# Optimization experiments

Measured on AMD Instinct MI355X. Metric: run time of the kernel, lower is better.

## Reference

```python
import jax, jax.numpy as jnp
import numpy as np

H = 2048          # hidden_size
DIN = 4096        # mamba intermediate (expand*H)
DS = 128          # ssm state size
DCONV = 4         # conv kernel
NH = 64           # ssm heads
HD = DIN // NH    # head dim = 64
NG = 1            # groups
FF = 8192         # mlp intermediate
EPS = 1e-5
B, L = 2, 2048
CONV_DIM = DIN + 2 * NG * DS            # 4352
D_IN_PROJ = 2 * DIN + 2 * NG * DS + NH  # 8512


def rmsnorm(x, w, eps=EPS):
    v = jnp.mean(jnp.square(x), axis=-1, keepdims=True)
    return x * jax.lax.rsqrt(v + eps) * w


def setup_inputs() -> dict:
    key = jax.random.key(0)
    ks = jax.random.split(key, 10)
    return {
        "hidden_states": jax.random.normal(ks[0], (B, L, H), jnp.float32),
        "w_in": 0.02 * jax.random.normal(ks[1], (H, D_IN_PROJ), jnp.float32),
        "conv_w": 0.1 * jax.random.normal(ks[2], (CONV_DIM, DCONV), jnp.float32),
        "conv_b": jnp.zeros((CONV_DIM,), jnp.float32),
        "A_log": jnp.log(1.0 + 15.0 * jax.random.uniform(ks[3], (NH,), jnp.float32)),
        "D_ssm": jnp.ones((NH,), jnp.float32),
        "dt_bias": 0.5 * jax.random.normal(ks[4], (NH,), jnp.float32),
        "norm_w": jnp.ones((DIN,), jnp.float32),
        "w_out": 0.02 * jax.random.normal(ks[5], (DIN, H), jnp.float32),
        "ln1_w": jnp.ones((H,), jnp.float32),
        "ln2_w": jnp.ones((H,), jnp.float32),
        "w_gate_up": 0.02 * jax.random.normal(ks[6], (H, 2 * FF), jnp.float32),
        "w_down": 0.02 * jax.random.normal(ks[7], (FF, H), jnp.float32),
    }


def mamba_mixer2(h, w_in, conv_w, conv_b, A_log, D_ssm, dt_bias, norm_w, w_out):
    # in_proj and split: [gate z | conv stream xBC | dt]
    proj = jnp.einsum('blh,hd->bld', h, w_in)
    z = proj[..., :DIN]
    xBC = proj[..., DIN:DIN + CONV_DIM]
    dt = proj[..., DIN + CONV_DIM:]                      # [B,L,NH]

    # causal depthwise conv over time, then silu
    kernel = conv_w.T[:, None, :]                        # [DCONV,1,CONV_DIM]
    xBC = jax.lax.conv_general_dilated(
        xBC, kernel, window_strides=(1,), padding=[(DCONV - 1, 0)],
        dimension_numbers=('NLC', 'LIO', 'NLC'), feature_group_count=CONV_DIM)
    xBC = jax.nn.silu(xBC + conv_b)

    x = xBC[..., :DIN].reshape(B, L, NH, HD)             # [B,L,NH,HD]
    Bc = xBC[..., DIN:DIN + NG * DS]                     # [B,L,DS] (NG=1)
    Cc = xBC[..., DIN + NG * DS:]                        # [B,L,DS]

    dt = jax.nn.softplus(dt + dt_bias)                   # [B,L,NH]
    A = -jnp.exp(A_log)                                  # [NH]
    dA = jnp.exp(dt * A)                                 # [B,L,NH]

    def step(hstate, inp):
        dA_t, dt_t, x_t, B_t, C_t = inp
        # hstate: [B,NH,HD,DS]
        hstate = (hstate * dA_t[:, :, None, None]
                  + (dt_t[:, :, None, None] * x_t[..., None]) * B_t[:, None, None, :])
        y_t = jnp.einsum('bhps,bs->bhp', hstate, C_t)
        return hstate, y_t

    h0 = jnp.zeros((B, NH, HD, DS), h.dtype)
    xs = (jnp.moveaxis(dA, 1, 0), jnp.moveaxis(dt, 1, 0), jnp.moveaxis(x, 1, 0),
          jnp.moveaxis(Bc, 1, 0), jnp.moveaxis(Cc, 1, 0))
    _, ys = jax.lax.scan(step, h0, xs)                   # ys: [L,B,NH,HD]
    y = jnp.moveaxis(ys, 0, 1) + D_ssm[None, None, :, None] * x
    y = y.reshape(B, L, DIN)

    # gated RMSNorm then out projection
    y = rmsnorm(y * jax.nn.silu(z), norm_w)
    return jnp.einsum('bld,dh->blh', y, w_out)


def reference(hidden_states, w_in, conv_w, conv_b, A_log, D_ssm, dt_bias,
              norm_w, w_out, ln1_w, ln2_w, w_gate_up, w_down):
    # residual is None on entry (first mamba layer path)
    residual = hidden_states
    h = rmsnorm(hidden_states, ln1_w)
    h = mamba_mixer2(h, w_in, conv_w, conv_b, A_log, D_ssm, dt_bias, norm_w, w_out)
    # fused add + norm
    residual = h + residual
    h = rmsnorm(residual, ln2_w)
    # SwiGLU MLP
    gu = jnp.einsum('blh,hf->blf', h, w_gate_up)
    h = jax.nn.silu(gu[..., :FF]) * gu[..., FF:]
    h = jnp.einsum('blf,fh->blh', h, w_down)
    return h, residual
```

## Files before the change

### kernel.cpp

```cpp
#include <hip/hip_runtime.h>
#include <hip/hip_bf16.h>
#include <stdint.h>

typedef __hip_bfloat16 bf16;
typedef __attribute__((ext_vector_type(8))) short bf16x8s;
typedef __attribute__((ext_vector_type(4))) float f32x4;
typedef __attribute__((ext_vector_type(8))) unsigned short us8;

#define DEV __device__ __forceinline__
#define MFMA16(a, b, c) __builtin_amdgcn_mfma_f32_16x16x32_bf16(a, b, c, 0, 0, 0)
#define AS1 __attribute__((address_space(1)))
#define AS3 __attribute__((address_space(3)))

static constexpr int Bn = 2, Ln = 2048, Hn = 2048, DINn = 4096, DSn = 128;
static constexpr int NHn = 64, FFn = 8192;
static constexpr int CONVD = DINn + 2 * DSn;
static constexpr int DPROJ = 2 * DINn + 2 * DSn + NHn;
static constexpr int DPROJP = 8704;
static constexpr int BL = Bn * Ln;
static constexpr int LC2 = 64, NCH = Ln / LC2;

DEV float bf2f(unsigned short x) {
  union { unsigned int u; float f; } v; v.u = ((unsigned int)x) << 16; return v.f;
}
DEV float bfload(const bf16* p) { return bf2f(*(const unsigned short*)p); }
DEV float sigmoidf_(float x) { return 1.f / (1.f + __expf(-x)); }

__global__ __launch_bounds__(256) void transpose_f2b_k(
    const float* __restrict__ in, bf16* __restrict__ out, int K, int N) {
  __shared__ bf16 t[32][33];
  int nb = blockIdx.x * 32, kb = blockIdx.y * 32;
  int tx = threadIdx.x & 31, ty = threadIdx.x >> 5;
#pragma unroll
  for (int r = 0; r < 32; r += 8)
    t[ty + r][tx] = __float2bfloat16(in[(size_t)(kb + ty + r) * N + nb + tx]);
  __syncthreads();
#pragma unroll
  for (int r = 0; r < 32; r += 8)
    out[(size_t)(nb + ty + r) * K + kb + tx] = t[tx][ty + r];
}

__global__ __launch_bounds__(256) void rmsnorm_f32_k(
    const float* __restrict__ in, const float* __restrict__ g, bf16* __restrict__ out) {
  int row = blockIdx.x, tid = threadIdx.x;
  const float* rp = in + (size_t)row * Hn + tid * 8;
  float4 a = *(const float4*)rp;
  float4 b = *(const float4*)(rp + 4);
  float v[8] = {a.x, a.y, a.z, a.w, b.x, b.y, b.z, b.w};
  float ss = 0.f;
#pragma unroll
  for (int j = 0; j < 8; ++j) ss += v[j] * v[j];
#pragma unroll
  for (int o = 1; o < 64; o <<= 1) ss += __shfl_xor(ss, o, 64);
  __shared__ float red[4];
  if ((tid & 63) == 0) red[tid >> 6] = ss;
  __syncthreads();
  float sc = rsqrtf((red[0] + red[1] + red[2] + red[3]) / Hn + 1e-5f);
  float4 g0 = *(const float4*)(g + tid * 8);
  float4 g1 = *(const float4*)(g + tid * 8 + 4);
  float gv[8] = {g0.x, g0.y, g0.z, g0.w, g1.x, g1.y, g1.z, g1.w};
  us8 ov;
#pragma unroll
  for (int j = 0; j < 8; ++j)
    ((bf16*)&ov)[j] = __float2bfloat16(v[j] * sc * gv[j]);
  *(us8*)(out + (size_t)row * Hn + tid * 8) = ov;
}

template<int MF, int EPI, typename OutT>
__global__ __launch_bounds__(512, (MF == 8 ? 2 : 4)) void gemm256_k(
    const bf16* __restrict__ A, const bf16* __restrict__ Bt,
    OutT* __restrict__ C, const float* __restrict__ Res,
    int K, int lda, int N, int nby) {
  constexpr int BM = MF * 32;
  __shared__ bf16 Abuf[3][BM * 32];
  __shared__ bf16 Bbuf[3][256 * 32];
  int nwg = gridDim.x;
  int orig = blockIdx.x;
  int wg = (orig & 7) * (nwg >> 3) + (orig >> 3);
  int by = wg % nby, bx = wg / nby;
  int m0 = by * BM, n0 = bx * 256;
  int tid = threadIdx.x;
  int lane = tid & 63, wid = tid >> 6;
  int wr = wid >> 2, wc = wid & 3;
  int l15 = lane & 15, l4 = lane >> 4;

  int P0 = tid * 16;
  int P1 = 8192 + tid * 16;
  int L0 = P0 ^ (((P0 >> 7) & 3) << 4);
  int L1 = P1 ^ (((P1 >> 7) & 3) << 4);
  int ar1 = (MF == 8) ? (L1 >> 6) : 0;
  const bf16* Ag0 = A + (size_t)(m0 + (L0 >> 6)) * lda + ((L0 >> 4) & 3) * 8;
  const bf16* Ag1 = A + (size_t)(m0 + ar1) * lda + ((L1 >> 4) & 3) * 8;
  const bf16* Bg0 = Bt + (size_t)(n0 + (L0 >> 6)) * K + ((L0 >> 4) & 3) * 8;
  const bf16* Bg1 = Bt + (size_t)(n0 + (L1 >> 6)) * K + ((L1 >> 4) & 3) * 8;

  auto stage = [&](int bi, int k0) {
    char* ab = (char*)&Abuf[bi][0];
    char* bb = (char*)&Bbuf[bi][0];
    __builtin_amdgcn_global_load_lds((const AS1 unsigned int*)(Ag0 + k0), (AS3 unsigned int*)(ab + P0), 16, 0, 0);
    if constexpr (MF == 8)
      __builtin_amdgcn_global_load_lds((const AS1 unsigned int*)(Ag1 + k0), (AS3 unsigned int*)(ab + P1), 16, 0, 0);
    __builtin_amdgcn_global_load_lds((const AS1 unsigned int*)(Bg0 + k0), (AS3 unsigned int*)(bb + P0), 16, 0, 0);
    __builtin_amdgcn_global_load_lds((const AS1 unsigned int*)(Bg1 + k0), (AS3 unsigned int*)(bb + P1), 16, 0, 0);
  };

  f32x4 acc[MF][4] = {};
  int arow0 = wr * (MF * 16) + l15;
  int acol = (l4 * 16) ^ (((arow0 >> 1) & 3) << 4);
  int brow0 = wc * 64 + l15;
  int bcol = (l4 * 16) ^ (((brow0 >> 1) & 3) << 4);
  int NT = K >> 5;

  stage(0, 0);
  stage(1, 32);
  if constexpr (MF == 8) asm volatile("s_waitcnt vmcnt(4)" ::: "memory");
  else                   asm volatile("s_waitcnt vmcnt(3)" ::: "memory");
  __builtin_amdgcn_s_barrier();
  asm volatile("" ::: "memory");

  for (int t = 0; t < NT; ++t) {
    const char* Ab = (const char*)&Abuf[t % 3][0];
    const char* Bb = (const char*)&Bbuf[t % 3][0];
    bf16x8s af[MF], bfv[4];
#pragma unroll
    for (int m = 0; m < MF; ++m)
      af[m] = *(const bf16x8s*)(Ab + (arow0 + m * 16) * 64 + acol);
#pragma unroll
    for (int n = 0; n < 4; ++n)
      bfv[n] = *(const bf16x8s*)(Bb + (brow0 + n * 16) * 64 + bcol);
    if (t + 2 < NT) stage((t + 2) % 3, (t + 2) * 32);
    __builtin_amdgcn_s_setprio(1);
#pragma unroll
    for (int m = 0; m < MF; ++m)
#pragma unroll
      for (int n = 0; n < 4; ++n)
        acc[m][n] = MFMA16(af[m], bfv[n], acc[m][n]);
    __builtin_amdgcn_s_setprio(0);
    if (t + 2 < NT) {
      if constexpr (MF == 8) asm volatile("s_waitcnt vmcnt(4)" ::: "memory");
      else                   asm volatile("s_waitcnt vmcnt(3)" ::: "memory");
    } else {
      asm volatile("s_waitcnt vmcnt(0)" ::: "memory");
    }
    __builtin_amdgcn_s_barrier();
    asm volatile("" ::: "memory");
  }

#pragma unroll
  for (int m = 0; m < MF; ++m) {
    int row = m0 + wr * (MF * 16) + m * 16 + l4 * 4;
#pragma unroll
    for (int n = 0; n < 4; ++n) {
      int col = n0 + wc * 64 + n * 16 + l15;
      if (col < N) {
#pragma unroll
        for (int r = 0; r < 4; ++r) {
          float vv = acc[m][n][r];
          if (EPI == 1) vv += Res[(size_t)(row + r) * N + col];
          if constexpr (__is_same(OutT, float)) C[(size_t)(row + r) * N + col] = vv;
          else C[(size_t)(row + r) * N + col] = __float2bfloat16(vv);
        }
      }
    }
  }
}

__global__ __launch_bounds__(256) void conv_silu_k(
    const bf16* __restrict__ proj, const float* __restrict__ cw,
    const float* __restrict__ cb, bf16* __restrict__ xb, bf16* __restrict__ bc) {
  int c = blockIdx.x * 256 + threadIdx.x;
  int bt = blockIdx.y;
  int l = bt & (Ln - 1);
  const bf16* base = proj + (size_t)bt * DPROJ + DINn + c;
  float acc = cb[c];
#pragma unroll
  for (int k = 0; k < 4; ++k) {
    int dl = l - 3 + k;
    if (dl >= 0) acc += bfload(base + (ptrdiff_t)(k - 3) * DPROJ) * cw[c * 4 + k];
  }
  float r = acc * sigmoidf_(acc);
  if (c < DINn) xb[(size_t)bt * DINn + c] = __float2bfloat16(r);
  else          bc[(size_t)bt * 256 + (c - DINn)] = __float2bfloat16(r);
}

__global__ __launch_bounds__(256) void dtda_k(
    const bf16* __restrict__ proj, const float* __restrict__ dt_bias,
    const float* __restrict__ A_log, float* __restrict__ dt, float* __restrict__ la) {
  int i = blockIdx.x * 256 + threadIdx.x;
  int bt = i >> 6, h = i & 63;
  float raw = bfload(proj + (size_t)bt * DPROJ + (DINn + CONVD) + h) + dt_bias[h];
  float dtv = raw > 20.f ? raw : log1pf(expf(raw));
  float Ah = -expf(A_log[h]);
  dt[i] = dtv;
  la[i] = dtv * Ah;
}

__global__ __launch_bounds__(256) void cumsum_k(
    const float* __restrict__ la, float* __restrict__ sarr) {
  int blk = blockIdx.x;
  int b = blk >> 6, h = blk & 63;
  int tid = threadIdx.x;
  int ch = tid >> 3, l8 = tid & 7;
  int t0 = ch * LC2 + l8 * 8;
  const float* lp = la + ((size_t)b * Ln + t0) * NHn + h;
  float v[8];
#pragma unroll
  for (int k = 0; k < 8; ++k) v[k] = lp[(size_t)k * NHn];
#pragma unroll
  for (int k = 1; k < 8; ++k) v[k] += v[k - 1];
  float tot = v[7];
  float run = tot;
#pragma unroll
  for (int d = 1; d < 8; d <<= 1) {
    float u = __shfl_up(run, d, 8);
    if (l8 >= d) run += u;
  }
  float excl = run - tot;
  float* out = sarr + (size_t)blk * Ln + t0;
#pragma unroll
  for (int k = 0; k < 8; ++k) out[k] = excl + v[k];
}

__global__ __launch_bounds__(256) void ssd1_k(
    const bf16* __restrict__ xb, const bf16* __restrict__ bc,
    const float* __restrict__ dtb, const float* __restrict__ sarr,
    bf16* __restrict__ ys, bf16* __restrict__ hend) {
  __shared__ bf16 Bs[64][136];
  __shared__ bf16 Cs[64][136];
  __shared__ bf16 BdT[128][72];
  __shared__ bf16 XTs[64][72];
  __shared__ bf16 Ss[64][72];
  __shared__ float sA[64];
  __shared__ float dts[64];
  int idx = blockIdx.x;
  int ch = idx & (NCH - 1), h = (idx >> 5) & 63, b = idx >> 11;
  int tid = threadIdx.x;
  size_t bt0 = (size_t)b * Ln + ch * LC2;
  if (tid < 64) {
    sA[tid] = sarr[(size_t)(b * 64 + h) * Ln + ch * LC2 + tid];
    dts[tid] = dtb[(bt0 + tid) * NHn + h];
  }
  __syncthreads();
  float sLast = sA[63];
  {
    int j = tid & 63, q = tid >> 6;
    float wj = dts[j] * __expf(sLast - sA[j]);
    const bf16* src = bc + (bt0 + j) * 256 + q * 64;
#pragma unroll
    for (int m8 = 0; m8 < 8; ++m8) {
      us8 v = *(const us8*)(src + m8 * 8);
      if (q < 2) {
        *(us8*)&Bs[j][q * 64 + m8 * 8] = v;
#pragma unroll
        for (int e = 0; e < 8; ++e)
          BdT[q * 64 + m8 * 8 + e][j] = __float2bfloat16(bf2f(v[e]) * wj);
      } else {
        *(us8*)&Cs[j][(q - 2) * 64 + m8 * 8] = v;
      }
    }
  }
  {
    int j = tid & 63, q = tid >> 6;
    const bf16* src = xb + (bt0 + j) * DINn + h * 64 + q * 16;
    us8 v0 = *(const us8*)src;
    us8 v1 = *(const us8*)(src + 8);
#pragma unroll
    for (int e = 0; e < 8; ++e) XTs[q * 16 + e][j] = *(const bf16*)&((unsigned short*)&v0)[e];
#pragma unroll
    for (int e = 0; e < 8; ++e) XTs[q * 16 + 8 + e][j] = *(const bf16*)&((unsigned short*)&v1)[e];
  }
  __syncthreads();
  int lane = tid & 63, wid = tid >> 6;
  int wr = wid >> 1, wc = wid & 1;
  int l15 = lane & 15, l4 = lane >> 4;
  f32x4 acc1[2][2] = {};
#pragma unroll
  for (int kk = 0; kk < 4; ++kk) {
    int kr = kk * 32 + l4 * 8;
    bf16x8s a0 = *(const bf16x8s*)&Cs[wr * 32 + l15][kr];
    bf16x8s a1 = *(const bf16x8s*)&Cs[wr * 32 + 16 + l15][kr];
    bf16x8s b0 = *(const bf16x8s*)&Bs[wc * 32 + l15][kr];
    bf16x8s b1 = *(const bf16x8s*)&Bs[wc * 32 + 16 + l15][kr];
    acc1[0][0] = MFMA16(a0, b0, acc1[0][0]);
    acc1[0][1] = MFMA16(a0, b1, acc1[0][1]);
    acc1[1][0] = MFMA16(a1, b0, acc1[1][0]);
    acc1[1][1] = MFMA16(a1, b1, acc1[1][1]);
  }
#pragma unroll
  for (int m = 0; m < 2; ++m)
#pragma unroll
    for (int n = 0; n < 2; ++n) {
      int j = wc * 32 + n * 16 + l15;
      float sj = sA[j], dj = dts[j];
#pragma unroll
      for (int r = 0; r < 4; ++r) {
        int i = wr * 32 + m * 16 + l4 * 4 + r;
        float val = (i >= j) ? __expf(sA[i] - sj) * acc1[m][n][r] * dj : 0.f;
        Ss[i][j] = __float2bfloat16(val);
      }
    }
  __syncthreads();
  f32x4 acc2[2][2] = {};
#pragma unroll
  for (int kk = 0; kk < 2; ++kk) {
    int kr = kk * 32 + l4 * 8;
    bf16x8s a0 = *(const bf16x8s*)&Ss[wr * 32 + l15][kr];
    bf16x8s a1 = *(const bf16x8s*)&Ss[wr * 32 + 16 + l15][kr];
    bf16x8s b0 = *(const bf16x8s*)&XTs[wc * 32 + l15][kr];
    bf16x8s b1 = *(const bf16x8s*)&XTs[wc * 32 + 16 + l15][kr];
    acc2[0][0] = MFMA16(a0, b0, acc2[0][0]);
    acc2[0][1] = MFMA16(a0, b1, acc2[0][1]);
    acc2[1][0] = MFMA16(a1, b0, acc2[1][0]);
    acc2[1][1] = MFMA16(a1, b1, acc2[1][1]);
  }
#pragma unroll
  for (int m = 0; m < 2; ++m)
#pragma unroll
    for (int n = 0; n < 2; ++n) {
      int p = wc * 32 + n * 16 + l15;
#pragma unroll
      for (int r = 0; r < 4; ++r) {
        int i = wr * 32 + m * 16 + l4 * 4 + r;
        ys[(bt0 + i) * DINn + h * 64 + p] = __float2bfloat16(acc2[m][n][r]);
      }
    }
  f32x4 acc3[2][4] = {};
#pragma unroll
  for (int kk = 0; kk < 2; ++kk) {
    int kr = kk * 32 + l4 * 8;
    bf16x8s a0 = *(const bf16x8s*)&XTs[wr * 32 + l15][kr];
    bf16x8s a1 = *(const bf16x8s*)&XTs[wr * 32 + 16 + l15][kr];
#pragma unroll
    for (int n = 0; n < 4; ++n) {
      bf16x8s bb = *(const bf16x8s*)&BdT[wc * 64 + n * 16 + l15][kr];
      acc3[0][n] = MFMA16(a0, bb, acc3[0][n]);
      acc3[1][n] = MFMA16(a1, bb, acc3[1][n]);
    }
  }
  bf16* hb = hend + ((size_t)((b * 64 + h) * NCH + ch)) * 8192;
#pragma unroll
  for (int m = 0; m < 2; ++m)
#pragma unroll
    for (int n = 0; n < 4; ++n) {
      int s = wc * 64 + n * 16 + l15;
#pragma unroll
      for (int r = 0; r < 4; ++r) {
        int p = wr * 32 + m * 16 + l4 * 4 + r;
        hb[p * 128 + s] = __float2bfloat16(acc3[m][n][r]);
      }
    }
}

__global__ __launch_bounds__(256) void carry_k(
    bf16* __restrict__ hend, const float* __restrict__ sarr) {
  int blk = blockIdx.x;
  int tid = threadIdx.x;
  bf16* base = hend + (size_t)blk * NCH * 8192 + tid * 32;
  const float* sp = sarr + (size_t)blk * Ln;
  float c[32];
#pragma unroll
  for (int i = 0; i < 32; ++i) c[i] = 0.f;
  for (int j = 0; j < NCH; ++j) {
    float aT = __expf(sp[j * LC2 + LC2 - 1]);
    bf16* pj = base + (size_t)j * 8192;
    float tmp[32];
#pragma unroll
    for (int q = 0; q < 4; ++q) {
      us8 v = ((const us8*)pj)[q];
#pragma unroll
      for (int e = 0; e < 8; ++e) tmp[q * 8 + e] = bf2f(v[e]);
    }
#pragma unroll
    for (int q = 0; q < 4; ++q) {
      us8 o;
#pragma unroll
      for (int e = 0; e < 8; ++e) ((bf16*)&o)[e] = __float2bfloat16(c[q * 8 + e]);
      ((us8*)pj)[q] = o;
    }
#pragma unroll
    for (int i = 0; i < 32; ++i) c[i] = fmaf(aT, c[i], tmp[i]);
  }
}

__global__ __launch_bounds__(256) void ssd2_k(
    const bf16* __restrict__ bc, const float* __restrict__ sarr,
    const bf16* __restrict__ hinit, bf16* __restrict__ ys) {
  __shared__ bf16 Ce[64][136];
  __shared__ bf16 Hs[64][136];
  __shared__ float sA[64];
  int idx = blockIdx.x;
  int ch = idx & (NCH - 1), h = (idx >> 5) & 63, b = idx >> 11;
  int tid = threadIdx.x;
  size_t bt0 = (size_t)b * Ln + ch * LC2;
  if (tid < 64) sA[tid] = sarr[(size_t)(b * 64 + h) * Ln + ch * LC2 + tid];
  __syncthreads();
  {
    int i = tid & 63, q = tid >> 6;
    float ei = __expf(sA[i]);
    const bf16* src = bc + (bt0 + i) * 256 + 128 + q * 32;
#pragma unroll
    for (int m8 = 0; m8 < 4; ++m8) {
      us8 v = *(const us8*)(src + m8 * 8);
      us8 o;
#pragma unroll
      for (int e = 0; e < 8; ++e) ((bf16*)&o)[e] = __float2bfloat16(bf2f(v[e]) * ei);
      *(us8*)&Ce[i][q * 32 + m8 * 8] = o;
    }
    const bf16* hsrc = hinit + ((size_t)((b * 64 + h) * NCH + ch)) * 8192 + i * 128 + q * 32;
#pragma unroll
    for (int m8 = 0; m8 < 4; ++m8)
      *(us8*)&Hs[i][q * 32 + m8 * 8] = *(const us8*)(hsrc + m8 * 8);
  }
  __syncthreads();
  int lane = tid & 63, wid = tid >> 6;
  int wr = wid >> 1, wc = wid & 1;
  int l15 = lane & 15, l4 = lane >> 4;
  f32x4 acc[2][2] = {};
#pragma unroll
  for (int kk = 0; kk < 4; ++kk) {
    int kr = kk * 32 + l4 * 8;
    bf16x8s a0 = *(const bf16x8s*)&Ce[wr * 32 + l15][kr];
    bf16x8s a1 = *(const bf16x8s*)&Ce[wr * 32 + 16 + l15][kr];
    bf16x8s b0 = *(const bf16x8s*)&Hs[wc * 32 + l15][kr];
    bf16x8s b1 = *(const bf16x8s*)&Hs[wc * 32 + 16 + l15][kr];
    acc[0][0] = MFMA16(a0, b0, acc[0][0]);
    acc[0][1] = MFMA16(a0, b1, acc[0][1]);
    acc[1][0] = MFMA16(a1, b0, acc[1][0]);
    acc[1][1] = MFMA16(a1, b1, acc[1][1]);
  }
#pragma unroll
  for (int m = 0; m < 2; ++m)
#pragma unroll
    for (int n = 0; n < 2; ++n) {
      int p = wc * 32 + n * 16 + l15;
#pragma unroll
      for (int r = 0; r < 4; ++r) {
        int i = wr * 32 + m * 16 + l4 * 4 + r;
        bf16* yy = &ys[(bt0 + i) * DINn + h * 64 + p];
        *yy = __float2bfloat16(bfload(yy) + acc[m][n][r]);
      }
    }
}

__global__ __launch_bounds__(256) void gated_norm_k(
    const bf16* __restrict__ ys, const bf16* __restrict__ xb,
    const float* __restrict__ Dp, const bf16* __restrict__ proj,
    const float* __restrict__ gw, bf16* __restrict__ out) {
  int row = blockIdx.x, tid = threadIdx.x;
  const bf16* yr = ys + (size_t)row * DINn;
  const bf16* xr = xb + (size_t)row * DINn;
  const bf16* zr = proj + (size_t)row * DPROJ;
  float v[2][8];
  float ss = 0.f;
#pragma unroll
  for (int it = 0; it < 2; ++it) {
    int base = (it * 256 + tid) * 8;
    float Dh = Dp[base >> 6];
    us8 y = *(const us8*)(yr + base);
    us8 x = *(const us8*)(xr + base);
    us8 z = *(const us8*)(zr + base);
#pragma unroll
    for (int j = 0; j < 8; ++j) {
      float zf = bf2f(z[j]);
      float val = (bf2f(y[j]) + Dh * bf2f(x[j])) * zf * sigmoidf_(zf);
      v[it][j] = val; ss += val * val;
    }
  }
#pragma unroll
  for (int o = 1; o < 64; o <<= 1) ss += __shfl_xor(ss, o, 64);
  __shared__ float red[4];
  if ((tid & 63) == 0) red[tid >> 6] = ss;
  __syncthreads();
  float sc = rsqrtf((red[0] + red[1] + red[2] + red[3]) / DINn + 1e-5f);
#pragma unroll
  for (int it = 0; it < 2; ++it) {
    int base = (it * 256 + tid) * 8;
    float4 g0 = *(const float4*)(gw + base);
    float4 g1 = *(const float4*)(gw + base + 4);
    float gv[8] = {g0.x, g0.y, g0.z, g0.w, g1.x, g1.y, g1.z, g1.w};
    us8 ov;
#pragma unroll
    for (int j = 0; j < 8; ++j)
      ((bf16*)&ov)[j] = __float2bfloat16(v[it][j] * sc * gv[j]);
    *(us8*)(out + (size_t)row * DINn + base) = ov;
  }
}

__global__ __launch_bounds__(256) void act_k(bf16* __restrict__ gu) {
  int i = blockIdx.x * 256 + threadIdx.x;
  int row = i >> 10, g = i & 1023;
  bf16* rp = gu + (size_t)row * (2 * FFn) + g * 8;
  us8 a = *(const us8*)(rp);
  us8 bx = *(const us8*)(rp + FFn);
  us8 ov;
#pragma unroll
  for (int j = 0; j < 8; ++j) {
    float av = bf2f(a[j]), bv = bf2f(bx[j]);
    ((bf16*)&ov)[j] = __float2bfloat16(av * sigmoidf_(av) * bv);
  }
  *(us8*)rp = ov;
}

extern "C" void kernel_launch(void* const* d_in, const int* in_sizes, int n_in,
                              void* d_out, int out_size, void* d_ws, size_t ws_size,
                              hipStream_t stream) {
  (void)in_sizes; (void)n_in; (void)out_size; (void)ws_size;
  const float* hidden  = (const float*)d_in[0];
  const float* w_in    = (const float*)d_in[1];
  const float* conv_w  = (const float*)d_in[2];
  const float* conv_b  = (const float*)d_in[3];
  const float* A_log   = (const float*)d_in[4];
  const float* D_ssm   = (const float*)d_in[5];
  const float* dt_bias = (const float*)d_in[6];
  const float* norm_w  = (const float*)d_in[7];
  const float* w_out   = (const float*)d_in[8];
  const float* ln1_w   = (const float*)d_in[9];
  const float* ln2_w   = (const float*)d_in[10];
  const float* w_gu    = (const float*)d_in[11];
  const float* w_dn    = (const float*)d_in[12];

  char* ws = (char*)d_ws;
  const size_t OFF_WT   = 0;
  const size_t OFF_PROJ = 67108864ull;
  const size_t OFF_XB   = OFF_PROJ + 69730304ull;
  const size_t OFF_BC   = OFF_XB  + 33554432ull;
  const size_t OFF_DTB  = OFF_BC  + 2097152ull;
  const size_t OFF_LA   = OFF_DTB + 1048576ull;
  const size_t OFF_SARR = OFF_LA  + 1048576ull;
  const size_t OFF_YS   = OFF_SARR + 1048576ull;
  const size_t OFF_YBF  = OFF_YS  + 33554432ull;
  const size_t OFF_HLN  = OFF_YBF + 33554432ull;
  const size_t OFF_HEND = OFF_WT;
  const size_t OFF_GU   = OFF_PROJ;

  bf16*  wT   = (bf16*)(ws + OFF_WT);
  bf16*  proj = (bf16*)(ws + OFF_PROJ);
  bf16*  xb   = (bf16*)(ws + OFF_XB);
  bf16*  bcb  = (bf16*)(ws + OFF_BC);
  float* dtb  = (float*)(ws + OFF_DTB);
  float* la   = (float*)(ws + OFF_LA);
  float* sarr = (float*)(ws + OFF_SARR);
  bf16*  ysb  = (bf16*)(ws + OFF_YS);
  bf16*  ybf  = (bf16*)(ws + OFF_YBF);
  bf16*  hln  = (bf16*)(ws + OFF_HLN);
  bf16*  hend = (bf16*)(ws + OFF_HEND);
  bf16*  gu   = (bf16*)(ws + OFF_GU);

  float* h_out = (float*)d_out;
  float* resid = h_out + (size_t)BL * Hn;

  transpose_f2b_k<<<dim3(DPROJ / 32, Hn / 32), 256, 0, stream>>>(w_in, wT, Hn, DPROJ);
  hipMemsetAsync(wT + (size_t)DPROJ * Hn, 0, (size_t)(DPROJP - DPROJ) * Hn * 2, stream);
  rmsnorm_f32_k<<<BL, 256, 0, stream>>>(hidden, ln1_w, hln);
  gemm256_k<8, 0, bf16><<<(DPROJP / 256) * (BL / 256), 512, 0, stream>>>(
      hln, wT, proj, nullptr, Hn, Hn, DPROJ, BL / 256);

  conv_silu_k<<<dim3(CONVD / 256, BL), 256, 0, stream>>>(proj, conv_w, conv_b, xb, bcb);
  dtda_k<<<BL * NHn / 256, 256, 0, stream>>>(proj, dt_bias, A_log, dtb, la);
  cumsum_k<<<Bn * NHn, 256, 0, stream>>>(la, sarr);

  ssd1_k<<<Bn * NHn * NCH, 256, 0, stream>>>(xb, bcb, dtb, sarr, ysb, hend);
  carry_k<<<Bn * NHn, 256, 0, stream>>>(hend, sarr);
  ssd2_k<<<Bn * NHn * NCH, 256, 0, stream>>>(bcb, sarr, hend, ysb);

  gated_norm_k<<<BL, 256, 0, stream>>>(ysb, xb, D_ssm, proj, norm_w, ybf);
  transpose_f2b_k<<<dim3(Hn / 32, DINn / 32), 256, 0, stream>>>(w_out, wT, DINn, Hn);
  gemm256_k<4, 1, float><<<(Hn / 256) * (BL / 128), 512, 0, stream>>>(
      ybf, wT, resid, hidden, DINn, DINn, Hn, BL / 128);

  rmsnorm_f32_k<<<BL, 256, 0, stream>>>(resid, ln2_w, hln);
  transpose_f2b_k<<<dim3(2 * FFn / 32, Hn / 32), 256, 0, stream>>>(w_gu, wT, Hn, 2 * FFn);
  gemm256_k<8, 0, bf16><<<(2 * FFn / 256) * (BL / 256), 512, 0, stream>>>(
      hln, wT, gu, nullptr, Hn, Hn, 2 * FFn, BL / 256);
  act_k<<<BL * FFn / 8 / 256, 256, 0, stream>>>(gu);
  transpose_f2b_k<<<dim3(Hn / 32, FFn / 32), 256, 0, stream>>>(w_dn, wT, FFn, Hn);
  gemm256_k<4, 0, float><<<(Hn / 256) * (BL / 128), 512, 0, stream>>>(
      gu, wT, h_out, nullptr, FFn, 2 * FFn, Hn, BL / 128);
}
```

Measured before the change: 1.048 ms.

## Add 256x256 GEMM with K=64 double-buffered, XOR-swizzled LDS and interleaved staging

Adds a new 256x256 tile GEMM kernel that loads K=64 slices into two LDS buffers split into half-tiles, using direct global-to-LDS loads and an XOR swizzle to avoid bank conflicts. Each K step is split into four MFMA quadrants, and the next tile's half-loads are issued between them so global traffic overlaps the matrix math. It replaces the triple-buffered K=32 kernel for the in_proj and gate_up GEMMs, the two largest bf16-output matmuls. It adds many barriers and depends on careful vmcnt accounting, so a counting mistake could cause races or stalls.

```diff
diff --git a/kernel.cpp b/kernel.cpp
--- a/kernel.cpp
+++ b/kernel.cpp
@@ -64,6 +64,152 @@
   for (int j = 0; j < 8; ++j)
     ((bf16*)&ov)[j] = __float2bfloat16(v[j] * sc * gv[j]);
   *(us8*)(out + (size_t)row * Hn + tid * 8) = ov;
+}
+
+template<int EPI, typename OutT>
+__global__ __launch_bounds__(512, 2) void gemm8p_k(
+    const bf16* __restrict__ A, const bf16* __restrict__ Bt,
+    OutT* __restrict__ C, const float* __restrict__ Res,
+    int K, int lda, int N, int nby) {
+  __shared__ bf16 Ab[2][2][128 * 64];
+  __shared__ bf16 Bb[2][2][128 * 64];
+  int nwg = gridDim.x;
+  int orig = blockIdx.x;
+  int wg = (orig & 7) * (nwg >> 3) + (orig >> 3);
+  int by = wg % nby, bx = wg / nby;
+  int m0 = by * 256, n0 = bx * 256;
+  int tid = threadIdx.x;
+  int lane = tid & 63, wid = tid >> 6;
+  int wr = wid >> 2, wc = wid & 3;
+  int l15 = lane & 15, l4 = lane >> 4;
+  int NT = K >> 6;
+
+  int P0 = tid * 16, P1 = tid * 16 + 8192;
+  int r0 = P0 >> 7, r1 = P1 >> 7;
+  int s0 = ((P0 >> 4) & 7) ^ (r0 & 7);
+  int s1 = ((P1 >> 4) & 7) ^ (r1 & 7);
+  const bf16* Ag[2][2];
+  const bf16* Bg[2][2];
+#pragma unroll
+  for (int h = 0; h < 2; ++h) {
+    Ag[h][0] = A + (size_t)(m0 + h * 128 + r0) * lda + s0 * 8;
+    Ag[h][1] = A + (size_t)(m0 + h * 128 + r1) * lda + s1 * 8;
+    Bg[h][0] = Bt + (size_t)(n0 + h * 128 + r0) * K + s0 * 8;
+    Bg[h][1] = Bt + (size_t)(n0 + h * 128 + r1) * K + s1 * 8;
+  }
+
+  auto stageA = [&](int t) {
+  };
+  (void)stageA;
+#define STAGE_A(hh, tt)                                                                  \
+  if ((tt) < NT) {                                                                       \
+    char* dst = (char*)&Ab[(tt) & 1][hh][0];                                             \
+    __builtin_amdgcn_global_load_lds((const AS1 unsigned int*)(Ag[hh][0] + (tt) * 64),   \
+                                     (AS3 unsigned int*)(dst + P0), 16, 0, 0);           \
+    __builtin_amdgcn_global_load_lds((const AS1 unsigned int*)(Ag[hh][1] + (tt) * 64),   \
+                                     (AS3 unsigned int*)(dst + P1), 16, 0, 0);           \
+  }
+#define STAGE_B(hh, tt)                                                                  \
+  if ((tt) < NT) {                                                                       \
+    char* dst = (char*)&Bb[(tt) & 1][hh][0];                                             \
+    __builtin_amdgcn_global_load_lds((const AS1 unsigned int*)(Bg[hh][0] + (tt) * 64),   \
+                                     (AS3 unsigned int*)(dst + P0), 16, 0, 0);           \
+    __builtin_amdgcn_global_load_lds((const AS1 unsigned int*)(Bg[hh][1] + (tt) * 64),   \
+                                     (AS3 unsigned int*)(dst + P1), 16, 0, 0);           \
+  }
+
+  f32x4 acc[8][4] = {};
+  bf16x8s af[4], bf[4];
+
+#define LDA_FRAG(i, mh, kk, d)                                                            \
+  {                                                                                       \
+    int rr = (mh) * 64 + (i) * 16 + l15;                                                  \
+    af[i] = *(const bf16x8s*)((const char*)&Ab[d][wr][0] + rr * 128 +                     \
+                              ((((kk) * 4 + l4) ^ (rr & 7)) << 4));                       \
+  }
+#define LDB_FRAG(n, kk, d)                                                                \
+  {                                                                                       \
+    int rr = (wc & 1) * 64 + (n) * 16 + l15;                                              \
+    bf[n] = *(const bf16x8s*)((const char*)&Bb[d][wc >> 1][0] + rr * 128 +                \
+                              ((((kk) * 4 + l4) ^ (rr & 7)) << 4));                       \
+  }
+#define MFMA_QUAD(mh, kk)                                                                 \
+  __builtin_amdgcn_s_setprio(1);                                                         \
+  _Pragma("unroll") for (int i = 0; i < 4; ++i) {                                        \
+    _Pragma("unroll") for (int n = 0; n < 4; ++n)                                        \
+        acc[(mh) * 4 + i][n] = MFMA16(af[i], bf[n], acc[(mh) * 4 + i][n]);               \
+  }                                                                                       \
+  __builtin_amdgcn_s_setprio(0);
+#define LGKM0                                                                             \
+  asm volatile("s_waitcnt lgkmcnt(0)" ::: "memory");                                      \
+  __builtin_amdgcn_sched_barrier(0);
+
+  STAGE_A(0, 0) STAGE_A(1, 0) STAGE_B(0, 0) STAGE_B(1, 0) STAGE_B(0, 1)
+  if (NT > 1) { asm volatile("s_waitcnt vmcnt(2)" ::: "memory"); }
+  else        { asm volatile("s_waitcnt vmcnt(0)" ::: "memory"); }
+  __builtin_amdgcn_s_barrier();
+
+  for (int t = 0; t < NT; ++t) {
+    const int d = t & 1;
+#pragma unroll
+    for (int i = 0; i < 4; ++i) LDA_FRAG(i, 0, 0, d)
+#pragma unroll
+    for (int n = 0; n < 4; ++n) LDB_FRAG(n, 0, d)
+    STAGE_B(1, t + 1)
+    __builtin_amdgcn_s_barrier();
+    LGKM0
+    MFMA_QUAD(0, 0)
+    __builtin_amdgcn_s_barrier();
+#pragma unroll
+    for (int i = 0; i < 4; ++i) LDA_FRAG(i, 1, 0, d)
+    STAGE_A(0, t + 1)
+    __builtin_amdgcn_s_barrier();
+    LGKM0
+    MFMA_QUAD(1, 0)
+    __builtin_amdgcn_s_barrier();
+#pragma unroll
+    for (int i = 0; i < 4; ++i) LDA_FRAG(i, 0, 1, d)
+#pragma unroll
+    for (int n = 0; n < 4; ++n) LDB_FRAG(n, 1, d)
+    STAGE_A(1, t + 1)
+    __builtin_amdgcn_s_barrier();
+    LGKM0
+    MFMA_QUAD(0, 1)
+    __builtin_amdgcn_s_barrier();
+#pragma unroll
+    for (int i = 0; i < 4; ++i) LDA_FRAG(i, 1, 1, d)
+    STAGE_B(0, t + 2)
+    __builtin_amdgcn_s_barrier();
+    LGKM0
+    MFMA_QUAD(1, 1)
+    if (t + 2 < NT) { asm volatile("s_waitcnt vmcnt(2)" ::: "memory"); }
+    else            { asm volatile("s_waitcnt vmcnt(0)" ::: "memory"); }
+    __builtin_amdgcn_s_barrier();
+  }
+
+#pragma unroll
+  for (int m = 0; m < 8; ++m) {
+    int row = m0 + wr * 128 + m * 16 + l4 * 4;
+#pragma unroll
+    for (int n = 0; n < 4; ++n) {
+      int col = n0 + wc * 64 + n * 16 + l15;
+      if (col < N) {
+#pragma unroll
+        for (int r = 0; r < 4; ++r) {
+          float vv = acc[m][n][r];
+          if (EPI == 1) vv += Res[(size_t)(row + r) * N + col];
+          if constexpr (__is_same(OutT, float)) C[(size_t)(row + r) * N + col] = vv;
+          else C[(size_t)(row + r) * N + col] = __float2bfloat16(vv);
+        }
+      }
+    }
+  }
+#undef STAGE_A
+#undef STAGE_B
+#undef LDA_FRAG
+#undef LDB_FRAG
+#undef MFMA_QUAD
+#undef LGKM0
 }
 
 template<int MF, int EPI, typename OutT>
@@ -552,7 +698,7 @@
   transpose_f2b_k<<<dim3(DPROJ / 32, Hn / 32), 256, 0, stream>>>(w_in, wT, Hn, DPROJ);
   hipMemsetAsync(wT + (size_t)DPROJ * Hn, 0, (size_t)(DPROJP - DPROJ) * Hn * 2, stream);
   rmsnorm_f32_k<<<BL, 256, 0, stream>>>(hidden, ln1_w, hln);
-  gemm256_k<8, 0, bf16><<<(DPROJP / 256) * (BL / 256), 512, 0, stream>>>(
+  gemm8p_k<0, bf16><<<(DPROJP / 256) * (BL / 256), 512, 0, stream>>>(
       hln, wT, proj, nullptr, Hn, Hn, DPROJ, BL / 256);
 
   conv_silu_k<<<dim3(CONVD / 256, BL), 256, 0, stream>>>(proj, conv_w, conv_b, xb, bcb);
@@ -570,7 +716,7 @@
 
   rmsnorm_f32_k<<<BL, 256, 0, stream>>>(resid, ln2_w, hln);
   transpose_f2b_k<<<dim3(2 * FFn / 32, Hn / 32), 256, 0, stream>>>(w_gu, wT, Hn, 2 * FFn);
-  gemm256_k<8, 0, bf16><<<(2 * FFn / 256) * (BL / 256), 512, 0, stream>>>(
+  gemm8p_k<0, bf16><<<(2 * FFn / 256) * (BL / 256), 512, 0, stream>>>(
       hln, wT, gu, nullptr, Hn, Hn, 2 * FFn, BL / 256);
   act_k<<<BL * FFn / 8 / 256, 256, 0, stream>>>(gu);
   transpose_f2b_k<<<dim3(Hn / 32, FFn / 32), 256, 0, stream>>>(w_dn, wT, FFn, Hn);
```

Result: no change. 1.069 ms (+1.9%).

## Add GEMM variant loading B fragments directly into registers, bypassing LDS

Applied to the files above, without the earlier changes.

Adds a 256x256 GEMM kernel that stages only the A tile through LDS with triple buffering. Each wave loads its B-operand fragments straight from global memory into registers, double-buffered across K steps. It is used for the in-projection and gate/up GEMMs. This halves LDS traffic and LDS footprint per block, but makes B loads uncoalesced across lanes (each lane reads 16 bytes from a different row) and repeats B reads across the two wave rows.

```diff
diff --git a/kernel.cpp b/kernel.cpp
--- a/kernel.cpp
+++ b/kernel.cpp
@@ -64,6 +64,118 @@
   for (int j = 0; j < 8; ++j)
     ((bf16*)&ov)[j] = __float2bfloat16(v[j] * sc * gv[j]);
   *(us8*)(out + (size_t)row * Hn + tid * 8) = ov;
+}
+
+template<int EPI, typename OutT>
+__global__ __launch_bounds__(512, 2) void gemmBreg_k(
+    const bf16* __restrict__ A, const bf16* __restrict__ Bt,
+    OutT* __restrict__ C, const float* __restrict__ Res,
+    int K, int lda, int N, int nby) {
+  __shared__ bf16 Abuf[3][256 * 32];
+  int nwg = gridDim.x;
+  int orig = blockIdx.x;
+  int wg = (orig & 7) * (nwg >> 3) + (orig >> 3);
+  int by = wg % nby, bx = wg / nby;
+  int m0 = by * 256, n0 = bx * 256;
+  int tid = threadIdx.x;
+  int lane = tid & 63, wid = tid >> 6;
+  int wr = wid >> 2, wc = wid & 3;
+  int l15 = lane & 15, l4 = lane >> 4;
+
+  int P0 = tid * 16;
+  int P1 = 8192 + tid * 16;
+  int L0 = P0 ^ (((P0 >> 7) & 3) << 4);
+  int L1 = P1 ^ (((P1 >> 7) & 3) << 4);
+  const bf16* Ag0 = A + (size_t)(m0 + (L0 >> 6)) * lda + ((L0 >> 4) & 3) * 8;
+  const bf16* Ag1 = A + (size_t)(m0 + (L1 >> 6)) * lda + ((L1 >> 4) & 3) * 8;
+
+  auto stageA = [&](int bi, int k0) {
+    char* ab = (char*)&Abuf[bi][0];
+    __builtin_amdgcn_global_load_lds((const AS1 unsigned int*)(Ag0 + k0), (AS3 unsigned int*)(ab + P0), 16, 0, 0);
+    __builtin_amdgcn_global_load_lds((const AS1 unsigned int*)(Ag1 + k0), (AS3 unsigned int*)(ab + P1), 16, 0, 0);
+  };
+
+  const bf16* Bp[4];
+#pragma unroll
+  for (int n = 0; n < 4; ++n)
+    Bp[n] = Bt + (size_t)(n0 + wc * 64 + n * 16 + l15) * K + l4 * 8;
+
+  f32x4 acc[8][4] = {};
+  int arow0 = wr * 128 + l15;
+  int acol = (l4 * 16) ^ (((arow0 >> 1) & 3) << 4);
+  int NT = K >> 5;
+
+  bf16x8s bA[4], bB[4], af[8];
+
+  stageA(0, 0);
+#pragma unroll
+  for (int n = 0; n < 4; ++n) bA[n] = *(const bf16x8s*)(Bp[n]);
+  stageA(1, 32);
+  asm volatile("s_waitcnt vmcnt(2)" ::: "memory");
+  __builtin_amdgcn_s_barrier();
+
+  for (int t = 0; t < NT; t += 2) {
+    {
+      const char* Ab = (const char*)&Abuf[t % 3][0];
+#pragma unroll
+      for (int m = 0; m < 8; ++m)
+        af[m] = *(const bf16x8s*)(Ab + (arow0 + m * 16) * 64 + acol);
+      if (t + 1 < NT) {
+#pragma unroll
+        for (int n = 0; n < 4; ++n) bB[n] = *(const bf16x8s*)(Bp[n] + (t + 1) * 32);
+      }
+      if (t + 2 < NT) stageA((t + 2) % 3, (t + 2) * 32);
+      __builtin_amdgcn_s_setprio(1);
+#pragma unroll
+      for (int m = 0; m < 8; ++m)
+#pragma unroll
+        for (int n = 0; n < 4; ++n)
+          acc[m][n] = MFMA16(af[m], bA[n], acc[m][n]);
+      __builtin_amdgcn_s_setprio(0);
+      if (t + 2 < NT) { asm volatile("s_waitcnt vmcnt(2)" ::: "memory"); }
+      else            { asm volatile("s_waitcnt vmcnt(0)" ::: "memory"); }
+      __builtin_amdgcn_s_barrier();
+    }
+    if (t + 1 < NT) {
+      const char* Ab = (const char*)&Abuf[(t + 1) % 3][0];
+#pragma unroll
+      for (int m = 0; m < 8; ++m)
+        af[m] = *(const bf16x8s*)(Ab + (arow0 + m * 16) * 64 + acol);
+      if (t + 2 < NT) {
+#pragma unroll
+        for (int n = 0; n < 4; ++n) bA[n] = *(const bf16x8s*)(Bp[n] + (t + 2) * 32);
+      }
+      if (t + 3 < NT) stageA((t + 3) % 3, (t + 3) * 32);
+      __builtin_amdgcn_s_setprio(1);
+#pragma unroll
+      for (int m = 0; m < 8; ++m)
+#pragma unroll
+        for (int n = 0; n < 4; ++n)
+          acc[m][n] = MFMA16(af[m], bB[n], acc[m][n]);
+      __builtin_amdgcn_s_setprio(0);
+      if (t + 3 < NT) { asm volatile("s_waitcnt vmcnt(2)" ::: "memory"); }
+      else            { asm volatile("s_waitcnt vmcnt(0)" ::: "memory"); }
+      __builtin_amdgcn_s_barrier();
+    }
+  }
+
+#pragma unroll
+  for (int m = 0; m < 8; ++m) {
+    int row = m0 + wr * 128 + m * 16 + l4 * 4;
+#pragma unroll
+    for (int n = 0; n < 4; ++n) {
+      int col = n0 + wc * 64 + n * 16 + l15;
+      if (col < N) {
+#pragma unroll
+        for (int r = 0; r < 4; ++r) {
+          float vv = acc[m][n][r];
+          if (EPI == 1) vv += Res[(size_t)(row + r) * N + col];
+          if constexpr (__is_same(OutT, float)) C[(size_t)(row + r) * N + col] = vv;
+          else C[(size_t)(row + r) * N + col] = __float2bfloat16(vv);
+        }
+      }
+    }
+  }
 }
 
 template<int MF, int EPI, typename OutT>
@@ -552,7 +664,7 @@
   transpose_f2b_k<<<dim3(DPROJ / 32, Hn / 32), 256, 0, stream>>>(w_in, wT, Hn, DPROJ);
   hipMemsetAsync(wT + (size_t)DPROJ * Hn, 0, (size_t)(DPROJP - DPROJ) * Hn * 2, stream);
   rmsnorm_f32_k<<<BL, 256, 0, stream>>>(hidden, ln1_w, hln);
-  gemm256_k<8, 0, bf16><<<(DPROJP / 256) * (BL / 256), 512, 0, stream>>>(
+  gemmBreg_k<0, bf16><<<(DPROJP / 256) * (BL / 256), 512, 0, stream>>>(
       hln, wT, proj, nullptr, Hn, Hn, DPROJ, BL / 256);
 
   conv_silu_k<<<dim3(CONVD / 256, BL), 256, 0, stream>>>(proj, conv_w, conv_b, xb, bcb);
@@ -570,7 +682,7 @@
 
   rmsnorm_f32_k<<<BL, 256, 0, stream>>>(resid, ln2_w, hln);
   transpose_f2b_k<<<dim3(2 * FFn / 32, Hn / 32), 256, 0, stream>>>(w_gu, wT, Hn, 2 * FFn);
-  gemm256_k<8, 0, bf16><<<(2 * FFn / 256) * (BL / 256), 512, 0, stream>>>(
+  gemmBreg_k<0, bf16><<<(2 * FFn / 256) * (BL / 256), 512, 0, stream>>>(
       hln, wT, gu, nullptr, Hn, Hn, 2 * FFn, BL / 256);
   act_k<<<BL * FFn / 8 / 256, 256, 0, stream>>>(gu);
   transpose_f2b_k<<<dim3(Hn / 32, FFn / 32), 256, 0, stream>>>(w_dn, wT, FFn, Hn);
```

Measured after the change: 1.311 ms. +25.0%, slower.
